# Kernel optimization log

Measured on AMD Instinct MI355X. Metric: run time of the kernel, lower is better.

## Reference

```python
import jax, jax.numpy as jnp
import numpy as np

N_NODES = 100000
N_EDGES = 1600000
D_IN = 64
D_HID = 64
N_CLS = 4


def setup_inputs() -> dict:
    key = jax.random.key(0)
    ks = jax.random.split(key, 8)
    s = lambda d: 1.0 / np.sqrt(d)
    return {
        "node_features": jax.random.normal(ks[0], (N_NODES, D_IN), jnp.float32),
        "edge_src": jax.random.randint(ks[1], (N_EDGES,), 0, N_NODES, jnp.int32),
        "edge_dst": jax.random.randint(ks[2], (N_EDGES,), 0, N_NODES, jnp.int32),
        "W_self1": jax.random.normal(ks[3], (D_IN, D_HID), jnp.float32) * s(D_IN),
        "b_self1": jnp.zeros((D_HID,), jnp.float32),
        "W_neigh1": jax.random.normal(ks[4], (D_IN, D_HID), jnp.float32) * s(D_IN),
        "W_self2": jax.random.normal(ks[5], (D_HID, N_CLS), jnp.float32) * s(D_HID),
        "b_self2": jnp.zeros((N_CLS,), jnp.float32),
        "W_neigh2": jax.random.normal(ks[6], (D_HID, N_CLS), jnp.float32) * s(D_HID),
    }


def _sage_mean(h, edge_src, edge_dst, W_self, b_self, W_neigh, n_nodes):
    # mean aggregation over in-neighbors: gather src feats, segment-sum by dst
    msg_sum = jax.ops.segment_sum(h[edge_src], edge_dst, num_segments=n_nodes)
    deg = jax.ops.segment_sum(
        jnp.ones_like(edge_dst, dtype=h.dtype), edge_dst, num_segments=n_nodes
    )
    h_neigh = msg_sum / jnp.maximum(deg, 1.0)[:, None]
    # DGL SAGEConv: fc_self (with bias) + fc_neigh (no bias)
    return h @ W_self + b_self + h_neigh @ W_neigh


def reference(node_features, edge_src, edge_dst, W_self1, b_self1, W_neigh1,
              W_self2, b_self2, W_neigh2):
    n = node_features.shape[0]
    h1 = jnp.tanh(_sage_mean(node_features, edge_src, edge_dst,
                             W_self1, b_self1, W_neigh1, n))
    logits = _sage_mean(h1, edge_src, edge_dst, W_self2, b_self2, W_neigh2, n)
    return logits
```

## Files before the change

### kernel.cpp

```cpp
#include <hip/hip_runtime.h>
#include <hip/hip_bf16.h>
#include <stdint.h>

typedef unsigned short u16;
typedef unsigned int   u32;
typedef __attribute__((ext_vector_type(8))) short bf16x8;
typedef __attribute__((ext_vector_type(4))) float f32x4;
typedef __attribute__((ext_vector_type(4))) int   i32x4;

#define MAXB 256
#define BKT_SHIFT 9
#define BKT_NODES 512
#define CAP 12288
#define POISON 0xAAAAAAAAu

__device__ __forceinline__ float bf2f(u16 u) { return __uint_as_float(((u32)u) << 16); }
__device__ __forceinline__ u16 f2bf(float f) {
    u32 u = __float_as_uint(f);
    u += 0x7FFFu + ((u >> 16) & 1u);
    return (u16)(u >> 16);
}
__device__ __forceinline__ int pkbf(float a, float b) {
    return (int)__builtin_amdgcn_perm(__float_as_uint(b), __float_as_uint(a), 0x07060302u);
}


__global__ __launch_bounds__(256) void k_front(const float* __restrict__ X,
                                               const float* __restrict__ Ws,
                                               const float* __restrict__ b1,
                                               const float* __restrict__ Wn,
                                               u16* __restrict__ Zb,
                                               u16* __restrict__ Y,
                                               int n, int gemmBlocks,
                                               const int* __restrict__ src,
                                               const int* __restrict__ dst,
                                               u32* __restrict__ gcur,
                                               u32* __restrict__ binned,
                                               int E, int chunk, int nb) {
    __shared__ u16 wl[64 * 132];
    __shared__ int h[MAXB], base[MAXB], lcur[MAXB];
    int t = threadIdx.x;

    if ((int)blockIdx.x >= gemmBlocks) {
        int blk = blockIdx.x - gemmBlocks;
        for (int i = t; i < nb; i += 256) h[i] = 0;
        __syncthreads();
        int beg = blk * chunk, end = min(beg + chunk, E);
        for (int i = beg + t; i < end; i += 256) atomicAdd(&h[dst[i] >> BKT_SHIFT], 1);
        __syncthreads();
        for (int i = t; i < nb; i += 256) {
            int c = h[i];
            base[i] = c ? (int)(atomicAdd(&gcur[i], (u32)c) - POISON) : 0;
            lcur[i] = 0;
        }
        __syncthreads();
        for (int i = beg + t; i < end; i += 256) {
            int d = dst[i], bk = d >> BKT_SHIFT;
            int p = base[bk] + atomicAdd(&lcur[bk], 1);
            if (p < CAP)
                binned[(size_t)bk * CAP + p] = ((u32)src[i] << BKT_SHIFT) | (u32)(d & (BKT_NODES - 1));
        }
        return;
    }

    for (int i = t; i < 8192; i += 256) {
        int k = i >> 7, c = i & 127;
        float w = (c < 64) ? Ws[k * 64 + c] : Wn[k * 64 + (c - 64)];
        wl[k * 132 + c] = f2bf(w);
    }
    __syncthreads();

    int wid = t >> 6, lane = t & 63;
    int lrow = lane & 15, lquad = lane >> 4;

    bf16x8 bfrag[8][2];
#pragma unroll
    for (int ct = 0; ct < 8; ct++)
#pragma unroll
        for (int kf = 0; kf < 2; kf++)
#pragma unroll
            for (int j = 0; j < 8; j++)
                bfrag[ct][kf][j] = (short)wl[(kf * 32 + lquad * 8 + j) * 132 + ct * 16 + lrow];

    float bias[4];
#pragma unroll
    for (int ct = 0; ct < 4; ct++) bias[ct] = b1[ct * 16 + lrow];

    int tile = blockIdx.x * 4 + wid;
    int tiles = n >> 4;
    if (tile >= tiles) return;
    int nb4 = tile << 4;

    const float* xp = X + (size_t)(nb4 + lrow) * 64 + lquad * 8;
    f32x4 x0 = *(const f32x4*)(xp);
    f32x4 x1 = *(const f32x4*)(xp + 4);
    f32x4 x2 = *(const f32x4*)(xp + 32);
    f32x4 x3 = *(const f32x4*)(xp + 36);
    i32x4 p0, p1;
    p0.x = pkbf(x0.x, x0.y); p0.y = pkbf(x0.z, x0.w);
    p0.z = pkbf(x1.x, x1.y); p0.w = pkbf(x1.z, x1.w);
    p1.x = pkbf(x2.x, x2.y); p1.y = pkbf(x2.z, x2.w);
    p1.z = pkbf(x3.x, x3.y); p1.w = pkbf(x3.z, x3.w);
    bf16x8 af0 = __builtin_bit_cast(bf16x8, p0);
    bf16x8 af1 = __builtin_bit_cast(bf16x8, p1);

    f32x4 acc[8];
#pragma unroll
    for (int ct = 0; ct < 8; ct++) {
        f32x4 c = {0.f, 0.f, 0.f, 0.f};
        c = __builtin_amdgcn_mfma_f32_16x16x32_bf16(af0, bfrag[ct][0], c, 0, 0, 0);
        c = __builtin_amdgcn_mfma_f32_16x16x32_bf16(af1, bfrag[ct][1], c, 0, 0, 0);
        acc[ct] = c;
    }

    int rbase = nb4 + lquad * 4;
#pragma unroll
    for (int ct = 0; ct < 4; ct++)
#pragma unroll
        for (int r = 0; r < 4; r++)
            Zb[(size_t)(rbase + r) * 64 + ct * 16 + lrow] = f2bf(acc[ct][r] + bias[ct]);
#pragma unroll
    for (int ct = 0; ct < 4; ct++)
#pragma unroll
        for (int r = 0; r < 4; r++)
            Y[(size_t)(rbase + r) * 64 + ct * 16 + lrow] = f2bf(acc[ct + 4][r]);
}


__global__ __launch_bounds__(512) void k_csr(const u32* __restrict__ binned,
                                             const u32* __restrict__ gcur,
                                             int* __restrict__ rpb,
                                             int* __restrict__ rpe,
                                             int* __restrict__ col, int n) {
    __shared__ int cnt[BKT_NODES];
    __shared__ int wsum[8], woff[8];
    int b = blockIdx.x, t = threadIdx.x;
    int total = min((int)(gcur[b] - POISON), CAP);
    const u32* bb = binned + (size_t)b * CAP;
    cnt[t] = 0;
    __syncthreads();
    for (int i = t; i < total; i += 512)
        atomicAdd(&cnt[bb[i] & (BKT_NODES - 1)], 1);
    __syncthreads();
    int v = cnt[t];
    int lane = t & 63, w = t >> 6;
    int incl = v;
#pragma unroll
    for (int o = 1; o < 64; o <<= 1) {
        int x = __shfl_up(incl, o, 64);
        if (lane >= o) incl += x;
    }
    if (lane == 63) wsum[w] = incl;
    __syncthreads();
    if (t == 0) {
        int run = 0;
#pragma unroll
        for (int i = 0; i < 8; i++) { woff[i] = run; run += wsum[i]; }
    }
    __syncthreads();
    int excl = incl - v + woff[w];
    int gnode = b * BKT_NODES + t;
    int cb = b * CAP;
    if (gnode < n) { rpb[gnode] = cb + excl; rpe[gnode] = cb + excl + v; }
    cnt[t] = excl;
    __syncthreads();
    for (int i = t; i < total; i += 512) {
        u32 e = bb[i];
        int p = atomicAdd(&cnt[e & (BKT_NODES - 1)], 1);
        col[cb + p] = (int)(e >> BKT_SHIFT);
    }
}


__global__ __launch_bounds__(256) void k_gather1f(const int* __restrict__ rpb,
                                                  const int* __restrict__ rpe,
                                                  const int* __restrict__ col,
                                                  const u16* __restrict__ Zb,
                                                  const u16* __restrict__ Y,
                                                  const float* __restrict__ Ws2,
                                                  const float* __restrict__ b2,
                                                  const float* __restrict__ Wn2,
                                                  float* __restrict__ P,
                                                  u16* __restrict__ Q, int n) {
    int t = threadIdx.x;
    int q = t >> 4, l = t & 15;
    float wr[4][8], bb[4];
#pragma unroll
    for (int j = 0; j < 4; j++) {
        f32x4 a = *(const f32x4*)(Ws2 + (4 * l + j) * 4);
        f32x4 c = *(const f32x4*)(Wn2 + (4 * l + j) * 4);
        wr[j][0] = a.x; wr[j][1] = a.y; wr[j][2] = a.z; wr[j][3] = a.w;
        wr[j][4] = c.x; wr[j][5] = c.y; wr[j][6] = c.z; wr[j][7] = c.w;
    }
#pragma unroll
    for (int c = 0; c < 4; c++) bb[c] = b2[c];

    int node = blockIdx.x * 16 + q;
    if (node >= n) return;
    int beg = rpb[node], end = rpe[node];
    float a0 = 0.f, a1 = 0.f, a2 = 0.f, a3 = 0.f;
    int e = beg;
    for (; e + 4 <= end; e += 4) {
        int s0 = col[e], s1 = col[e + 1], s2 = col[e + 2], s3 = col[e + 3];
        ushort4 r0 = *(const ushort4*)(Y + (size_t)s0 * 64 + l * 4);
        ushort4 r1 = *(const ushort4*)(Y + (size_t)s1 * 64 + l * 4);
        ushort4 r2 = *(const ushort4*)(Y + (size_t)s2 * 64 + l * 4);
        ushort4 r3 = *(const ushort4*)(Y + (size_t)s3 * 64 + l * 4);
        a0 += bf2f(r0.x) + bf2f(r1.x) + bf2f(r2.x) + bf2f(r3.x);
        a1 += bf2f(r0.y) + bf2f(r1.y) + bf2f(r2.y) + bf2f(r3.y);
        a2 += bf2f(r0.z) + bf2f(r1.z) + bf2f(r2.z) + bf2f(r3.z);
        a3 += bf2f(r0.w) + bf2f(r1.w) + bf2f(r2.w) + bf2f(r3.w);
    }
    for (; e < end; e++) {
        ushort4 r = *(const ushort4*)(Y + (size_t)col[e] * 64 + l * 4);
        a0 += bf2f(r.x); a1 += bf2f(r.y); a2 += bf2f(r.z); a3 += bf2f(r.w);
    }
    float deg = (float)(end - beg);
    float inv = (deg > 0.f) ? 1.f / deg : 0.f;
    ushort4 z = *(const ushort4*)(Zb + (size_t)node * 64 + l * 4);
    float h0 = tanhf(bf2f(z.x) + a0 * inv);
    float h1 = tanhf(bf2f(z.y) + a1 * inv);
    float h2 = tanhf(bf2f(z.z) + a2 * inv);
    float h3 = tanhf(bf2f(z.w) + a3 * inv);

    float r[8];
#pragma unroll
    for (int c = 0; c < 8; c++)
        r[c] = h0 * wr[0][c] + h1 * wr[1][c] + h2 * wr[2][c] + h3 * wr[3][c];
#pragma unroll
    for (int m = 1; m < 16; m <<= 1)
#pragma unroll
        for (int c = 0; c < 8; c++) r[c] += __shfl_xor(r[c], m, 64);

    if (l == 0) {
        *(float4*)(P + (size_t)node * 4) =
            make_float4(r[0] + bb[0], r[1] + bb[1], r[2] + bb[2], r[3] + bb[3]);
        ushort4 qv;
        qv.x = f2bf(r[4]); qv.y = f2bf(r[5]); qv.z = f2bf(r[6]); qv.w = f2bf(r[7]);
        *(ushort4*)(Q + (size_t)node * 4) = qv;
    }
}


__global__ __launch_bounds__(256) void k_gather2(const int* __restrict__ rpb,
                                                 const int* __restrict__ rpe,
                                                 const int* __restrict__ col,
                                                 const float* __restrict__ P,
                                                 const u16* __restrict__ Q,
                                                 float* __restrict__ out, int n) {
    int node = blockIdx.x * 256 + threadIdx.x;
    if (node >= n) return;
    int beg = rpb[node], end = rpe[node];
    float a0 = 0.f, a1 = 0.f, a2 = 0.f, a3 = 0.f;
    int e = beg;
    for (; e + 4 <= end; e += 4) {
        int s0 = col[e], s1 = col[e + 1], s2 = col[e + 2], s3 = col[e + 3];
        ushort4 q0 = *(const ushort4*)(Q + (size_t)s0 * 4);
        ushort4 q1 = *(const ushort4*)(Q + (size_t)s1 * 4);
        ushort4 q2 = *(const ushort4*)(Q + (size_t)s2 * 4);
        ushort4 q3 = *(const ushort4*)(Q + (size_t)s3 * 4);
        a0 += bf2f(q0.x) + bf2f(q1.x) + bf2f(q2.x) + bf2f(q3.x);
        a1 += bf2f(q0.y) + bf2f(q1.y) + bf2f(q2.y) + bf2f(q3.y);
        a2 += bf2f(q0.z) + bf2f(q1.z) + bf2f(q2.z) + bf2f(q3.z);
        a3 += bf2f(q0.w) + bf2f(q1.w) + bf2f(q2.w) + bf2f(q3.w);
    }
    for (; e < end; e++) {
        ushort4 qv = *(const ushort4*)(Q + (size_t)col[e] * 4);
        a0 += bf2f(qv.x); a1 += bf2f(qv.y); a2 += bf2f(qv.z); a3 += bf2f(qv.w);
    }
    float deg = (float)(end - beg);
    float inv = (deg > 0.f) ? 1.f / deg : 0.f;
    float4 p = *(const float4*)(P + (size_t)node * 4);
    float4 o = make_float4(p.x + a0 * inv, p.y + a1 * inv,
                           p.z + a2 * inv, p.w + a3 * inv);
    *(float4*)(out + (size_t)node * 4) = o;
}


extern "C" void kernel_launch(void* const* d_in, const int* in_sizes, int n_in,
                              void* d_out, int out_size, void* d_ws, size_t ws_size,
                              hipStream_t stream) {
    const float* X   = (const float*)d_in[0];
    const int* esrc  = (const int*)d_in[1];
    const int* edst  = (const int*)d_in[2];
    const float* Ws1 = (const float*)d_in[3];
    const float* b1  = (const float*)d_in[4];
    const float* Wn1 = (const float*)d_in[5];
    const float* Ws2 = (const float*)d_in[6];
    const float* b2  = (const float*)d_in[7];
    const float* Wn2 = (const float*)d_in[8];
    float* out = (float*)d_out;

    const int n = in_sizes[0] / 64;
    const int E = in_sizes[1];
    const int nb = (n + BKT_NODES - 1) >> BKT_SHIFT;

    size_t off = 0;
    char* base = (char*)d_ws;
    auto give = [&](size_t bytes) -> char* {
        char* p = base + off;
        off += (bytes + 255) & ~(size_t)255;
        return p;
    };
    u32*   gcur   = (u32*)give((size_t)MAXB * 4);
    int*   rpb    = (int*)give((size_t)n * 4);
    int*   rpe    = (int*)give((size_t)n * 4);
    u32*   binned = (u32*)give((size_t)nb * CAP * 4);
    int*   col    = (int*)give((size_t)nb * CAP * 4);
    u16*   Zb     = (u16*)give((size_t)n * 64 * 2);
    u16*   Y      = (u16*)give((size_t)n * 64 * 2);
    float* P      = (float*)give((size_t)n * 4 * 4);
    u16*   Q      = (u16*)give((size_t)n * 4 * 2);

    int tiles = n >> 4;
    int gemmBlocks = (tiles + 3) / 4;
    const int binBlocks = 1024;
    const int chunk = (E + binBlocks - 1) / binBlocks;
    k_front<<<gemmBlocks + binBlocks, 256, 0, stream>>>(
        X, Ws1, b1, Wn1, Zb, Y, n, gemmBlocks,
        esrc, edst, gcur, binned, E, chunk, nb);

    k_csr<<<nb, 512, 0, stream>>>(binned, gcur, rpb, rpe, col, n);

    k_gather1f<<<(n + 15) / 16, 256, 0, stream>>>(rpb, rpe, col, Zb, Y,
                                                  Ws2, b2, Wn2, P, Q, n);
    k_gather2<<<(n + 255) / 256, 256, 0, stream>>>(rpb, rpe, col, P, Q, out, n);
}
```

Baseline: 191.4 us.

## Store neighbor projection in FP8 and reorder binning blocks first with fewer bins

The per-node neighbor projection Y, which is gathered once per edge, is now stored in FP8 (e4m3) instead of bf16. This halves the bytes fetched in the layer-1 gather, and the values are unpacked with hardware cvt_pk_f32_fp8. The edge-binning blocks now come first in the fused front kernel, and their count drops from 1024 to 192, so each block handles a larger chunk with fewer global atomics. The cost is lower precision in the aggregated messages, which risks tolerance failures.

```diff
diff --git a/kernel.cpp b/kernel.cpp
--- a/kernel.cpp
+++ b/kernel.cpp
@@ -2,9 +2,11 @@
 #include <hip/hip_bf16.h>
 #include <stdint.h>
 
+typedef unsigned char  u8;
 typedef unsigned short u16;
 typedef unsigned int   u32;
 typedef __attribute__((ext_vector_type(8))) short bf16x8;
+typedef __attribute__((ext_vector_type(2))) float f32x2;
 typedef __attribute__((ext_vector_type(4))) float f32x4;
 typedef __attribute__((ext_vector_type(4))) int   i32x4;
 
@@ -13,6 +15,7 @@
 #define BKT_NODES 512
 #define CAP 12288
 #define POISON 0xAAAAAAAAu
+#define BINBLK 192
 
 __device__ __forceinline__ float bf2f(u16 u) { return __uint_as_float(((u32)u) << 16); }
 __device__ __forceinline__ u16 f2bf(float f) {
@@ -23,6 +26,10 @@
 __device__ __forceinline__ int pkbf(float a, float b) {
     return (int)__builtin_amdgcn_perm(__float_as_uint(b), __float_as_uint(a), 0x07060302u);
 }
+__device__ __forceinline__ u8 f2fp8(float v) {
+    int p = __builtin_amdgcn_cvt_pk_fp8_f32(v, v, 0, false);
+    return (u8)(p & 0xff);
+}
 
 
 __global__ __launch_bounds__(256) void k_front(const float* __restrict__ X,
@@ -30,8 +37,8 @@
                                                const float* __restrict__ b1,
                                                const float* __restrict__ Wn,
                                                u16* __restrict__ Zb,
-                                               u16* __restrict__ Y,
-                                               int n, int gemmBlocks,
+                                               u8* __restrict__ Y,
+                                               int n,
                                                const int* __restrict__ src,
                                                const int* __restrict__ dst,
                                                u32* __restrict__ gcur,
@@ -41,8 +48,8 @@
     __shared__ int h[MAXB], base[MAXB], lcur[MAXB];
     int t = threadIdx.x;
 
-    if ((int)blockIdx.x >= gemmBlocks) {
-        int blk = blockIdx.x - gemmBlocks;
+    if ((int)blockIdx.x < BINBLK) {
+        int blk = blockIdx.x;
         for (int i = t; i < nb; i += 256) h[i] = 0;
         __syncthreads();
         int beg = blk * chunk, end = min(beg + chunk, E);
@@ -86,7 +93,7 @@
 #pragma unroll
     for (int ct = 0; ct < 4; ct++) bias[ct] = b1[ct * 16 + lrow];
 
-    int tile = blockIdx.x * 4 + wid;
+    int tile = (blockIdx.x - BINBLK) * 4 + wid;
     int tiles = n >> 4;
     if (tile >= tiles) return;
     int nb4 = tile << 4;
@@ -123,7 +130,7 @@
     for (int ct = 0; ct < 4; ct++)
 #pragma unroll
         for (int r = 0; r < 4; r++)
-            Y[(size_t)(rbase + r) * 64 + ct * 16 + lrow] = f2bf(acc[ct + 4][r]);
+            Y[(size_t)(rbase + r) * 64 + ct * 16 + lrow] = f2fp8(acc[ct + 4][r]);
 }
 
 
@@ -176,7 +183,7 @@
                                                   const int* __restrict__ rpe,
                                                   const int* __restrict__ col,
                                                   const u16* __restrict__ Zb,
-                                                  const u16* __restrict__ Y,
+                                                  const u8* __restrict__ Y,
                                                   const float* __restrict__ Ws2,
                                                   const float* __restrict__ b2,
                                                   const float* __restrict__ Wn2,
@@ -202,18 +209,23 @@
     int e = beg;
     for (; e + 4 <= end; e += 4) {
         int s0 = col[e], s1 = col[e + 1], s2 = col[e + 2], s3 = col[e + 3];
-        ushort4 r0 = *(const ushort4*)(Y + (size_t)s0 * 64 + l * 4);
-        ushort4 r1 = *(const ushort4*)(Y + (size_t)s1 * 64 + l * 4);
-        ushort4 r2 = *(const ushort4*)(Y + (size_t)s2 * 64 + l * 4);
-        ushort4 r3 = *(const ushort4*)(Y + (size_t)s3 * 64 + l * 4);
-        a0 += bf2f(r0.x) + bf2f(r1.x) + bf2f(r2.x) + bf2f(r3.x);
-        a1 += bf2f(r0.y) + bf2f(r1.y) + bf2f(r2.y) + bf2f(r3.y);
-        a2 += bf2f(r0.z) + bf2f(r1.z) + bf2f(r2.z) + bf2f(r3.z);
-        a3 += bf2f(r0.w) + bf2f(r1.w) + bf2f(r2.w) + bf2f(r3.w);
+        u32 y0 = *(const u32*)(Y + (size_t)s0 * 64 + l * 4);
+        u32 y1 = *(const u32*)(Y + (size_t)s1 * 64 + l * 4);
+        u32 y2 = *(const u32*)(Y + (size_t)s2 * 64 + l * 4);
+        u32 y3 = *(const u32*)(Y + (size_t)s3 * 64 + l * 4);
+#pragma unroll
+        for (int j = 0; j < 4; j++) {
+            u32 yw = (j == 0) ? y0 : (j == 1) ? y1 : (j == 2) ? y2 : y3;
+            f32x2 lo = __builtin_amdgcn_cvt_pk_f32_fp8(yw, false);
+            f32x2 hi = __builtin_amdgcn_cvt_pk_f32_fp8(yw, true);
+            a0 += lo.x; a1 += lo.y; a2 += hi.x; a3 += hi.y;
+        }
     }
     for (; e < end; e++) {
-        ushort4 r = *(const ushort4*)(Y + (size_t)col[e] * 64 + l * 4);
-        a0 += bf2f(r.x); a1 += bf2f(r.y); a2 += bf2f(r.z); a3 += bf2f(r.w);
+        u32 yw = *(const u32*)(Y + (size_t)col[e] * 64 + l * 4);
+        f32x2 lo = __builtin_amdgcn_cvt_pk_f32_fp8(yw, false);
+        f32x2 hi = __builtin_amdgcn_cvt_pk_f32_fp8(yw, true);
+        a0 += lo.x; a1 += lo.y; a2 += hi.x; a3 += hi.y;
     }
     float deg = (float)(end - beg);
     float inv = (deg > 0.f) ? 1.f / deg : 0.f;
@@ -308,16 +320,15 @@
     u32*   binned = (u32*)give((size_t)nb * CAP * 4);
     int*   col    = (int*)give((size_t)nb * CAP * 4);
     u16*   Zb     = (u16*)give((size_t)n * 64 * 2);
-    u16*   Y      = (u16*)give((size_t)n * 64 * 2);
+    u8*    Y      = (u8*)give((size_t)n * 64);
     float* P      = (float*)give((size_t)n * 4 * 4);
     u16*   Q      = (u16*)give((size_t)n * 4 * 2);
 
     int tiles = n >> 4;
     int gemmBlocks = (tiles + 3) / 4;
-    const int binBlocks = 1024;
-    const int chunk = (E + binBlocks - 1) / binBlocks;
-    k_front<<<gemmBlocks + binBlocks, 256, 0, stream>>>(
-        X, Ws1, b1, Wn1, Zb, Y, n, gemmBlocks,
+    const int chunk = (E + BINBLK - 1) / BINBLK;
+    k_front<<<BINBLK + gemmBlocks, 256, 0, stream>>>(
+        X, Ws1, b1, Wn1, Zb, Y, n,
         esrc, edst, gcur, binned, E, chunk, nb);
 
     k_csr<<<nb, 512, 0, stream>>>(binned, gcur, rpb, rpe, col, n);
```

Result: faster. 186.1 us (-2.8%).
